# Kernel tuning notes

Hardware: AMD Instinct MI355X
Metric: run time of the kernel (lower is better)

## Reference

```python
import jax, jax.numpy as jnp
import numpy as np
from jax import lax

COEF = 0.97  # rnn.weight_hh_l0; weight_ih_l0 == 1.0


def setup_inputs() -> dict:
    key = jax.random.key(0)
    B, C, T = 128, 1, 262144
    x = jax.random.normal(key, (B, C, T), dtype=jnp.float32)
    return {"input": x}


def reference(input) -> jnp.ndarray:
    # torch.nn.RNN(1,1,1,bias=False) with weight_ih=1, weight_hh=COEF and
    # default nonlinearity='tanh':  h[t] = tanh(x[t] + COEF * h[t-1])
    x = input[:, 0, :]                     # [B, T]
    B = x.shape[0]

    def step(h, x_t):                      # h: [B], x_t: [B]
        h = jnp.tanh(x_t + COEF * h)
        return h, h

    h0 = jnp.zeros((B,), dtype=x.dtype)
    _, ys = lax.scan(step, h0, x.T)        # ys: [T, B]
    return ys.T[:, None, :]                # [B, 1, T]
```

## Files before the change

### kernel.cpp

```cpp
#include <hip/hip_runtime.h>


#define BB 128
#define TT 262144
#define CHL 32
#define WW 64
#define WPR 128
#define NBLK ((BB * WPR) / 2)

typedef float f32x4 __attribute__((ext_vector_type(4)));

__device__ __forceinline__ int swq(int q) { return q ^ ((q >> 3) & 7); }

__global__ __launch_bounds__(128) void ipe_kernel(const float* __restrict__ x,
                                                  float* __restrict__ y) {
    const int lane = threadIdx.x & 63;
    const int wv   = threadIdx.x >> 6;
    const int bid  = (blockIdx.x & 7) * (NBLK >> 3) + (blockIdx.x >> 3);
    const int w    = bid * 2 + wv;
    const int row  = w >> 7;
    const int g    = w & (WPR - 1);
    const size_t rowBase = (size_t)row * TT;
    const long   t0 = (long)g * (64 * CHL);

    __shared__ float tile_all[2][528 * 4];
    float* tile = tile_all[wv];

    f32x4 pf[8], ph;
    #pragma unroll
    for (int m = 0; m < 8; ++m)
        pf[m] = *reinterpret_cast<const f32x4*>(x + rowBase + t0 + 256 * m + 4 * lane);
    if (lane < 16) {
        const long T = t0 - WW + 4 * lane;
        if (T >= 0) ph = *reinterpret_cast<const f32x4*>(x + rowBase + T);
        else        ph = (f32x4){0.f, 0.f, 0.f, 0.f};
    }

    #pragma unroll
    for (int m = 0; m < 8; ++m)
        *reinterpret_cast<f32x4*>(&tile[4 * swq(16 + 64 * m + lane)]) = pf[m];
    if (lane < 16)
        *reinterpret_cast<f32x4*>(&tile[4 * swq(lane)]) = ph;
    asm volatile("" ::: "memory");

    float xv[32];
    #pragma unroll
    for (int t = 0; t < 8; ++t) {
        f32x4 v = *reinterpret_cast<const f32x4*>(&tile[4 * swq(8 * lane + t)]);
        xv[4 * t + 0] = v.x; xv[4 * t + 1] = v.y;
        xv[4 * t + 2] = v.z; xv[4 * t + 3] = v.w;
    }
    #pragma unroll
    for (int t = 0; t < 8; ++t)
        pf[t] = *reinterpret_cast<const f32x4*>(&tile[4 * swq(8 * lane + 8 + t)]);

    const float C2 = 2.885390081777926815f;
    const float K2 = 0.97f * C2;
    float h = 0.f;

    #pragma unroll
    for (int k = 0; k < 32; ++k) {
        float z2 = fmaf(K2, h, xv[k] * C2);
        float ez = __builtin_amdgcn_exp2f(z2);
        float rc = __builtin_amdgcn_rcpf(ez + 1.0f);
        h = fmaf(-2.0f, rc, 1.0f);
    }

    #pragma unroll
    for (int t = 0; t < 8; ++t) {
        f32x4 v = *reinterpret_cast<const f32x4*>(&tile[4 * swq(16 + 8 * lane + t)]);
        xv[4 * t + 0] = v.x; xv[4 * t + 1] = v.y;
        xv[4 * t + 2] = v.z; xv[4 * t + 3] = v.w;
    }

    #pragma unroll
    for (int t = 0; t < 8; ++t) {
        float z2, ez, rc;
        z2 = fmaf(K2, h, pf[t].x * C2); ez = __builtin_amdgcn_exp2f(z2);
        rc = __builtin_amdgcn_rcpf(ez + 1.0f); h = fmaf(-2.0f, rc, 1.0f);
        z2 = fmaf(K2, h, pf[t].y * C2); ez = __builtin_amdgcn_exp2f(z2);
        rc = __builtin_amdgcn_rcpf(ez + 1.0f); h = fmaf(-2.0f, rc, 1.0f);
        z2 = fmaf(K2, h, pf[t].z * C2); ez = __builtin_amdgcn_exp2f(z2);
        rc = __builtin_amdgcn_rcpf(ez + 1.0f); h = fmaf(-2.0f, rc, 1.0f);
        z2 = fmaf(K2, h, pf[t].w * C2); ez = __builtin_amdgcn_exp2f(z2);
        rc = __builtin_amdgcn_rcpf(ez + 1.0f); h = fmaf(-2.0f, rc, 1.0f);
    }

    #pragma unroll
    for (int k = 0; k < 32; ++k) {
        float z2 = fmaf(K2, h, xv[k] * C2);
        float ez = __builtin_amdgcn_exp2f(z2);
        float rc = __builtin_amdgcn_rcpf(ez + 1.0f);
        h = fmaf(-2.0f, rc, 1.0f);
        xv[k] = h;
    }

    asm volatile("" ::: "memory");
    #pragma unroll
    for (int t = 0; t < 8; ++t) {
        f32x4 v;
        v.x = xv[4 * t + 0]; v.y = xv[4 * t + 1];
        v.z = xv[4 * t + 2]; v.w = xv[4 * t + 3];
        *reinterpret_cast<f32x4*>(&tile[4 * swq(16 + 8 * lane + t)]) = v;
    }
    asm volatile("" ::: "memory");

    #pragma unroll
    for (int m = 0; m < 8; ++m) {
        f32x4 v = *reinterpret_cast<const f32x4*>(&tile[4 * swq(16 + 64 * m + lane)]);
        *reinterpret_cast<f32x4*>(y + rowBase + t0 + 256 * m + 4 * lane) = v;
    }
}

extern "C" void kernel_launch(void* const* d_in, const int* in_sizes, int n_in,
                              void* d_out, int out_size, void* d_ws, size_t ws_size,
                              hipStream_t stream) {
    const float* x = (const float*)d_in[0];
    float* y = (float*)d_out;
    ipe_kernel<<<dim3(NBLK), dim3(128), 0, stream>>>(x, y);
}
```

Baseline: 46.22 us.

## Make waves loop over multiple regions with double-buffered register prefetch

The grid shrinks from one 2048-element region per wave to 16 waves per row. Each wave now walks 8 consecutive regions and prefetches the next region's global loads into registers while it computes the current one. The aim is to hide global-load latency and cut launch and wave-startup overhead. In exchange, far fewer waves are resident to hide the latency of the serial exp/rcp recurrence, register pressure rises from holding two prefetch buffers, and the XCD-aware block swizzle is removed.

```diff
diff --git a/kernel.cpp b/kernel.cpp
--- a/kernel.cpp
+++ b/kernel.cpp
@@ -3,9 +3,9 @@
 
 #define BB 128
 #define TT 262144
-#define CHL 32
-#define WW 64
-#define WPR 128
+#define REG 2048
+#define WPR 16
+#define RPW ((TT / REG) / WPR)
 #define NBLK ((BB * WPR) / 2)
 
 typedef float f32x4 __attribute__((ext_vector_type(4)));
@@ -16,99 +16,113 @@
                                                   float* __restrict__ y) {
     const int lane = threadIdx.x & 63;
     const int wv   = threadIdx.x >> 6;
-    const int bid  = (blockIdx.x & 7) * (NBLK >> 3) + (blockIdx.x >> 3);
-    const int w    = bid * 2 + wv;
-    const int row  = w >> 7;
-    const int g    = w & (WPR - 1);
+    const int w    = blockIdx.x * 2 + wv;
+    const int row  = w >> 4;
+    const int p    = w & 15;
     const size_t rowBase = (size_t)row * TT;
-    const long   t0 = (long)g * (64 * CHL);
+    const long   base = (long)p * (RPW * REG);
 
     __shared__ float tile_all[2][528 * 4];
     float* tile = tile_all[wv];
 
-    f32x4 pf[8], ph;
-    #pragma unroll
-    for (int m = 0; m < 8; ++m)
-        pf[m] = *reinterpret_cast<const f32x4*>(x + rowBase + t0 + 256 * m + 4 * lane);
-    if (lane < 16) {
-        const long T = t0 - WW + 4 * lane;
-        if (T >= 0) ph = *reinterpret_cast<const f32x4*>(x + rowBase + T);
-        else        ph = (f32x4){0.f, 0.f, 0.f, 0.f};
-    }
-
-    #pragma unroll
-    for (int m = 0; m < 8; ++m)
-        *reinterpret_cast<f32x4*>(&tile[4 * swq(16 + 64 * m + lane)]) = pf[m];
-    if (lane < 16)
-        *reinterpret_cast<f32x4*>(&tile[4 * swq(lane)]) = ph;
-    asm volatile("" ::: "memory");
-
-    float xv[32];
-    #pragma unroll
-    for (int t = 0; t < 8; ++t) {
-        f32x4 v = *reinterpret_cast<const f32x4*>(&tile[4 * swq(8 * lane + t)]);
-        xv[4 * t + 0] = v.x; xv[4 * t + 1] = v.y;
-        xv[4 * t + 2] = v.z; xv[4 * t + 3] = v.w;
-    }
-    #pragma unroll
-    for (int t = 0; t < 8; ++t)
-        pf[t] = *reinterpret_cast<const f32x4*>(&tile[4 * swq(8 * lane + 8 + t)]);
-
     const float C2 = 2.885390081777926815f;
     const float K2 = 0.97f * C2;
-    float h = 0.f;
 
-    #pragma unroll
-    for (int k = 0; k < 32; ++k) {
-        float z2 = fmaf(K2, h, xv[k] * C2);
-        float ez = __builtin_amdgcn_exp2f(z2);
-        float rc = __builtin_amdgcn_rcpf(ez + 1.0f);
-        h = fmaf(-2.0f, rc, 1.0f);
-    }
+    f32x4 pfA[8], phA, pfB[8], phB;
 
-    #pragma unroll
-    for (int t = 0; t < 8; ++t) {
-        f32x4 v = *reinterpret_cast<const f32x4*>(&tile[4 * swq(16 + 8 * lane + t)]);
-        xv[4 * t + 0] = v.x; xv[4 * t + 1] = v.y;
-        xv[4 * t + 2] = v.z; xv[4 * t + 3] = v.w;
-    }
+    auto load = [&](f32x4 (&pf)[8], f32x4& ph, long t0) {
+        #pragma unroll
+        for (int m = 0; m < 8; ++m)
+            pf[m] = *reinterpret_cast<const f32x4*>(x + rowBase + t0 + 256 * m + 4 * lane);
+        if (lane < 16) {
+            const long T = t0 - 64 + 4 * lane;
+            if (T >= 0) ph = *reinterpret_cast<const f32x4*>(x + rowBase + T);
+            else        ph = (f32x4){0.f, 0.f, 0.f, 0.f};
+        }
+    };
 
-    #pragma unroll
-    for (int t = 0; t < 8; ++t) {
-        float z2, ez, rc;
-        z2 = fmaf(K2, h, pf[t].x * C2); ez = __builtin_amdgcn_exp2f(z2);
-        rc = __builtin_amdgcn_rcpf(ez + 1.0f); h = fmaf(-2.0f, rc, 1.0f);
-        z2 = fmaf(K2, h, pf[t].y * C2); ez = __builtin_amdgcn_exp2f(z2);
-        rc = __builtin_amdgcn_rcpf(ez + 1.0f); h = fmaf(-2.0f, rc, 1.0f);
-        z2 = fmaf(K2, h, pf[t].z * C2); ez = __builtin_amdgcn_exp2f(z2);
-        rc = __builtin_amdgcn_rcpf(ez + 1.0f); h = fmaf(-2.0f, rc, 1.0f);
-        z2 = fmaf(K2, h, pf[t].w * C2); ez = __builtin_amdgcn_exp2f(z2);
-        rc = __builtin_amdgcn_rcpf(ez + 1.0f); h = fmaf(-2.0f, rc, 1.0f);
-    }
+    auto process = [&](f32x4 (&pf)[8], f32x4& ph, long t0) {
+        #pragma unroll
+        for (int m = 0; m < 8; ++m)
+            *reinterpret_cast<f32x4*>(&tile[4 * swq(16 + 64 * m + lane)]) = pf[m];
+        if (lane < 16)
+            *reinterpret_cast<f32x4*>(&tile[4 * swq(lane)]) = ph;
+        asm volatile("" ::: "memory");
 
-    #pragma unroll
-    for (int k = 0; k < 32; ++k) {
-        float z2 = fmaf(K2, h, xv[k] * C2);
-        float ez = __builtin_amdgcn_exp2f(z2);
-        float rc = __builtin_amdgcn_rcpf(ez + 1.0f);
-        h = fmaf(-2.0f, rc, 1.0f);
-        xv[k] = h;
-    }
+        float xv[32];
+        f32x4 pw[8];
+        #pragma unroll
+        for (int t = 0; t < 8; ++t) {
+            f32x4 v = *reinterpret_cast<const f32x4*>(&tile[4 * swq(8 * lane + t)]);
+            xv[4 * t + 0] = v.x; xv[4 * t + 1] = v.y;
+            xv[4 * t + 2] = v.z; xv[4 * t + 3] = v.w;
+        }
+        #pragma unroll
+        for (int t = 0; t < 8; ++t)
+            pw[t] = *reinterpret_cast<const f32x4*>(&tile[4 * swq(8 * lane + 8 + t)]);
 
-    asm volatile("" ::: "memory");
-    #pragma unroll
-    for (int t = 0; t < 8; ++t) {
-        f32x4 v;
-        v.x = xv[4 * t + 0]; v.y = xv[4 * t + 1];
-        v.z = xv[4 * t + 2]; v.w = xv[4 * t + 3];
-        *reinterpret_cast<f32x4*>(&tile[4 * swq(16 + 8 * lane + t)]) = v;
-    }
-    asm volatile("" ::: "memory");
+        float h = 0.f;
+        #pragma unroll
+        for (int k = 0; k < 32; ++k) {
+            float z2 = fmaf(K2, h, xv[k] * C2);
+            float ez = __builtin_amdgcn_exp2f(z2);
+            float rc = __builtin_amdgcn_rcpf(ez + 1.0f);
+            h = fmaf(-2.0f, rc, 1.0f);
+        }
 
-    #pragma unroll
-    for (int m = 0; m < 8; ++m) {
-        f32x4 v = *reinterpret_cast<const f32x4*>(&tile[4 * swq(16 + 64 * m + lane)]);
-        *reinterpret_cast<f32x4*>(y + rowBase + t0 + 256 * m + 4 * lane) = v;
+        #pragma unroll
+        for (int t = 0; t < 8; ++t) {
+            f32x4 v = *reinterpret_cast<const f32x4*>(&tile[4 * swq(16 + 8 * lane + t)]);
+            xv[4 * t + 0] = v.x; xv[4 * t + 1] = v.y;
+            xv[4 * t + 2] = v.z; xv[4 * t + 3] = v.w;
+        }
+
+        #pragma unroll
+        for (int t = 0; t < 8; ++t) {
+            float z2, ez, rc;
+            z2 = fmaf(K2, h, pw[t].x * C2); ez = __builtin_amdgcn_exp2f(z2);
+            rc = __builtin_amdgcn_rcpf(ez + 1.0f); h = fmaf(-2.0f, rc, 1.0f);
+            z2 = fmaf(K2, h, pw[t].y * C2); ez = __builtin_amdgcn_exp2f(z2);
+            rc = __builtin_amdgcn_rcpf(ez + 1.0f); h = fmaf(-2.0f, rc, 1.0f);
+            z2 = fmaf(K2, h, pw[t].z * C2); ez = __builtin_amdgcn_exp2f(z2);
+            rc = __builtin_amdgcn_rcpf(ez + 1.0f); h = fmaf(-2.0f, rc, 1.0f);
+            z2 = fmaf(K2, h, pw[t].w * C2); ez = __builtin_amdgcn_exp2f(z2);
+            rc = __builtin_amdgcn_rcpf(ez + 1.0f); h = fmaf(-2.0f, rc, 1.0f);
+        }
+
+        #pragma unroll
+        for (int k = 0; k < 32; ++k) {
+            float z2 = fmaf(K2, h, xv[k] * C2);
+            float ez = __builtin_amdgcn_exp2f(z2);
+            float rc = __builtin_amdgcn_rcpf(ez + 1.0f);
+            h = fmaf(-2.0f, rc, 1.0f);
+            xv[k] = h;
+        }
+
+        asm volatile("" ::: "memory");
+        #pragma unroll
+        for (int t = 0; t < 8; ++t) {
+            f32x4 v;
+            v.x = xv[4 * t + 0]; v.y = xv[4 * t + 1];
+            v.z = xv[4 * t + 2]; v.w = xv[4 * t + 3];
+            *reinterpret_cast<f32x4*>(&tile[4 * swq(16 + 8 * lane + t)]) = v;
+        }
+        asm volatile("" ::: "memory");
+        #pragma unroll
+        for (int m = 0; m < 8; ++m) {
+            f32x4 v = *reinterpret_cast<const f32x4*>(&tile[4 * swq(16 + 64 * m + lane)]);
+            *reinterpret_cast<f32x4*>(y + rowBase + t0 + 256 * m + 4 * lane) = v;
+        }
+        asm volatile("" ::: "memory");
+    };
+
+    load(pfA, phA, base);
+    #pragma unroll 1
+    for (int rr = 0; rr < RPW; rr += 2) {
+        load(pfB, phB, base + (long)(rr + 1) * REG);
+        process(pfA, phA, base + (long)rr * REG);
+        if (rr + 2 < RPW) load(pfA, phA, base + (long)(rr + 2) * REG);
+        process(pfB, phB, base + (long)(rr + 1) * REG);
     }
 }
 
```

Result: slower. 49.20 us (+6.5%).
